# Kernel tuning notes

Measured on AMD Instinct MI355X. Metric: run time of the kernel, lower is better.

Reference implementation:

```python
import jax, jax.numpy as jnp
import numpy as np
from jax import lax

EPS = 1e-8
DIL = 4  # 2**(dilation-1) with dilation=3


def prelu(x, a):
    return jnp.where(x >= 0, x, a * x)


def cln(x):
    # cumulative layer norm over (channels, causal time window); gamma=1, beta=0
    # x: [B, M, L]
    M = x.shape[1]
    L = x.shape[2]
    cnt = (M * jnp.arange(1, L + 1, dtype=x.dtype))  # [L]
    csum = jnp.cumsum(jnp.sum(x, axis=1), axis=-1)           # [B, L]
    csq = jnp.cumsum(jnp.sum(x * x, axis=1), axis=-1)        # [B, L]
    mean = csum / cnt                                         # [B, L]
    var = csq / cnt - mean * mean                             # [B, L]
    return (x - mean[:, None, :]) / jnp.sqrt(var[:, None, :] + EPS)


def depthwise_conv(x, dw, db):
    # x: [B, H, L]; dw: [H, 1, P]; grouped conv, groups=H, 'same' padding, dilation DIL
    y = lax.conv_general_dilated(
        x, dw,
        window_strides=(1,),
        padding='SAME',
        rhs_dilation=(DIL,),
        dimension_numbers=('NCH', 'OIH', 'NCH'),
        feature_group_count=x.shape[1],
    )
    return y + db[None, :, None]


def setup_inputs() -> dict:
    key = jax.random.key(0)
    ks = jax.random.split(key, 9)
    Bc, H, P, Sc = 128, 512, 3, 128
    bsz, L = 4, 8000
    return {
        'x': jax.random.normal(ks[0], (bsz, Bc, L), dtype=jnp.float32),
        'W1': jax.random.normal(ks[1], (H, Bc), dtype=jnp.float32) * 0.05,
        'b1': jax.random.normal(ks[2], (H,), dtype=jnp.float32) * 0.02,
        'dw': jax.random.normal(ks[3], (H, 1, P), dtype=jnp.float32) * 0.1,
        'db': jax.random.normal(ks[4], (H,), dtype=jnp.float32) * 0.02,
        'Wout': jax.random.normal(ks[5], (Bc, H), dtype=jnp.float32) * 0.05,
        'bout': jax.random.normal(ks[6], (Bc,), dtype=jnp.float32) * 0.02,
        'Wskip': jax.random.normal(ks[7], (Sc, H), dtype=jnp.float32) * 0.05,
        'bskip': jax.random.normal(ks[8], (Sc,), dtype=jnp.float32) * 0.02,
        'a1': jnp.full((1,), 0.25, dtype=jnp.float32),
        'a2': jnp.full((1,), 0.25, dtype=jnp.float32),
    }


def reference(x, W1, b1, dw, db, Wout, bout, Wskip, bskip, a1, a2):
    res_x = x
    h = jnp.einsum('bcl,hc->bhl', x, W1) + b1[None, :, None]   # conv1x1 (k=1)
    h = prelu(h, a1)
    h = cln(h)
    h = depthwise_conv(h, dw, db)
    h = prelu(h, a2)
    h = cln(h)
    out = jnp.einsum('bhl,ch->bcl', h, Wout) + bout[None, :, None] + res_x
    skip = jnp.einsum('bhl,sh->bsl', h, Wskip) + bskip[None, :, None]
    return (out, skip)
```

## Files before the change

### kernel.cpp

```cpp
#include <hip/hip_runtime.h>

typedef unsigned short u16;
typedef unsigned int u32;
typedef __attribute__((ext_vector_type(8))) short bf16x8;
typedef __attribute__((ext_vector_type(4))) float f32x4;

#define Bn 4
#define Cn 128
#define Hn 512
#define Ln 8000
#define EPSf 1e-8f

__device__ __forceinline__ float bf2f(u32 v) { return __uint_as_float(v << 16); }
__device__ __forceinline__ u32 f2bf(float f) {
  u32 u = __float_as_uint(f);
  return (u + 0x7fffu + ((u >> 16) & 1u)) >> 16;
}
__device__ __forceinline__ void gl16(const void* g, void* l) {
  __builtin_amdgcn_global_load_lds((const __attribute__((address_space(1))) u32*)g,
                                   (__attribute__((address_space(3))) u32*)l, 16, 0, 0);
}

__global__ void k0_prep(const float* __restrict__ W1, const float* __restrict__ Wout,
                        const float* __restrict__ Wskip,
                        u16* __restrict__ W1b, u16* __restrict__ Wcatb,
                        float* __restrict__ Wsum)
{
  const int bid = blockIdx.x, tid = threadIdx.x;
  if (bid < 64) {
    const int base = (bid * 256 + tid) * 4;
#pragma unroll
    for (int t = 0; t < 4; ++t) {
      int i = base + t;
      int h = i >> 7, k = i & 127;
      int dbyte = h * 256 + (((k * 2) ^ ((h & 7) << 4)));
      W1b[dbyte >> 1] = (u16)f2bf(W1[h * Cn + k]);
    }
  } else if (bid < 192) {
    const int base = ((bid - 64) * 256 + tid) * 4;
#pragma unroll
    for (int t = 0; t < 4; ++t) {
      int j = base + t;
      int kt = j >> 14, r = j & 16383, c = r >> 6, kk = r & 63;
      int k = kt * 64 + kk;
      float v = (c < Cn) ? Wout[c * Hn + k] : Wskip[(c - Cn) * Hn + k];
      int dbyte = kt * 32768 + c * 128 + (((kk * 2) ^ ((c & 7) << 4)));
      Wcatb[dbyte >> 1] = (u16)f2bf(v);
    }
  } else {
    const int c = tid;
    const float* Wp = (c < Cn) ? (Wout + (size_t)c * Hn) : (Wskip + (size_t)(c - Cn) * Hn);
    float s = 0.f;
    for (int k = 0; k < Hn; ++k) s += Wp[k];
    Wsum[c] = s;
  }
}

__global__ __launch_bounds__(256, 2)
void k1_fused(const float* __restrict__ x, const u16* __restrict__ W1b,
              const float* __restrict__ b1, const float* __restrict__ a1p,
              u16* __restrict__ hT, float* __restrict__ sum1, float* __restrict__ sumsq1)
{
  __shared__ char regA[32768];
  __shared__ char xs[16384];
  __shared__ char stg[16384];
  __shared__ float b1s[512];
  const int bidx = blockIdx.x;
  const int b = bidx / 125, l0 = (bidx % 125) * 64;
  const int tid = threadIdx.x, ln = tid & 63, w = tid >> 6;
  const int ln15 = ln & 15, lq = ln >> 4;

  {
    const char* xb = (const char*)x + ((size_t)b * Cn * Ln + l0) * 4;
#pragma unroll
    for (int i = 0; i < 8; ++i) {
      int chunk = w * 8 + i;
      gl16(xb + (size_t)(chunk * 4 + (ln >> 4)) * (Ln * 4) + (ln & 15) * 16,
           regA + chunk * 1024);
    }
  }
  b1s[tid] = b1[tid];
  b1s[tid + 256] = b1[tid + 256];
  __syncthreads();
#pragma unroll
  for (int p = 0; p < 4; ++p) {
    int u = tid + p * 256;
    int l = u & 63, ui = u >> 6;
    u32 pk[4];
#pragma unroll
    for (int pp = 0; pp < 4; ++pp) {
      int c0 = ui * 8 + pp * 2;
      float f0 = *(const float*)(regA + c0 * 256 + l * 4);
      float f1 = *(const float*)(regA + (c0 + 1) * 256 + l * 4);
      pk[pp] = f2bf(f0) | (f2bf(f1) << 16);
    }
    uint4 st; st.x = pk[0]; st.y = pk[1]; st.z = pk[2]; st.w = pk[3];
    *(uint4*)(xs + l * 256 + ((ui * 16) ^ ((l & 7) << 4))) = st;
  }

  const float a1v = a1p[0];
  float sAcc = 0.f, qAcc = 0.f;

  for (int s = 0; s < 4; ++s) {
    __syncthreads();
#pragma unroll
    for (int i = 0; i < 8; ++i) {
      int chunk = w * 8 + i;
      gl16((const char*)W1b + s * 32768 + chunk * 1024 + ln * 16, regA + chunk * 1024);
    }
    __syncthreads();

    f32x4 acc[8];
    const f32x4 z4 = {0.f, 0.f, 0.f, 0.f};
#pragma unroll
    for (int rf = 0; rf < 8; ++rf) acc[rf] = z4;
#pragma unroll
    for (int kf = 0; kf < 4; ++kf) {
      const int brow = w * 16 + ln15;
      bf16x8 bfr = *(const bf16x8*)(xs + brow * 256 +
                                    ((kf * 64 + lq * 16) ^ ((brow & 7) << 4)));
#pragma unroll
      for (int rf = 0; rf < 8; ++rf) {
        int arow = rf * 16 + ln15;
        bf16x8 afr = *(const bf16x8*)(regA + arow * 256 +
                                      ((kf * 64 + lq * 16) ^ ((arow & 7) << 4)));
        acc[rf] = __builtin_amdgcn_mfma_f32_16x16x32_bf16(afr, bfr, acc[rf], 0, 0, 0);
      }
    }
#pragma unroll
    for (int rf = 0; rf < 8; ++rf) {
      int hb = s * 128 + rf * 16 + lq * 4;
      float v0 = acc[rf][0] + b1s[hb + 0]; v0 = v0 >= 0.f ? v0 : a1v * v0;
      float v1 = acc[rf][1] + b1s[hb + 1]; v1 = v1 >= 0.f ? v1 : a1v * v1;
      float v2 = acc[rf][2] + b1s[hb + 2]; v2 = v2 >= 0.f ? v2 : a1v * v2;
      float v3 = acc[rf][3] + b1s[hb + 3]; v3 = v3 >= 0.f ? v3 : a1v * v3;
      sAcc += v0 + v1 + v2 + v3;
      qAcc += v0 * v0 + v1 * v1 + v2 * v2 + v3 * v3;
      uint2 st2;
      st2.x = f2bf(v0) | (f2bf(v1) << 16);
      st2.y = f2bf(v2) | (f2bf(v3) << 16);
      *(uint2*)(stg + w * 4096 + ln15 * 256 +
                ((rf * 32 + lq * 8) ^ ((ln15 & 3) << 4))) = st2;
    }
#pragma unroll
    for (int p = 0; p < 4; ++p) {
      int lr = p * 4 + (ln >> 4);
      int j = ln & 15;
      uint4 v = *(const uint4*)(stg + w * 4096 + lr * 256 + ((j * 16) ^ ((lr & 3) << 4)));
      *(uint4*)((char*)hT + ((size_t)(b * Ln + l0 + w * 16 + lr)) * 1024 +
                s * 256 + j * 16) = v;
    }
  }
  sAcc += __shfl_xor(sAcc, 16); qAcc += __shfl_xor(qAcc, 16);
  sAcc += __shfl_xor(sAcc, 32); qAcc += __shfl_xor(qAcc, 32);
  if (lq == 0) {
    sum1[b * Ln + l0 + w * 16 + ln15] = sAcc;
    sumsq1[b * Ln + l0 + w * 16 + ln15] = qAcc;
  }
}

__global__ void k2_scan(const float* __restrict__ sum, const float* __restrict__ sumsq,
                        float* __restrict__ mean, float* __restrict__ rstd)
{
  const int b = blockIdx.x, tid = threadIdx.x;
  const int lane = tid & 63, w = tid >> 6;
  __shared__ float wts[4], wtq[4];
  float v[32], q[32];
  float ts = 0.f, tq = 0.f;
  const int base = tid * 32;
  const bool act = (tid < 250);
  if (act) {
#pragma unroll
    for (int i = 0; i < 8; ++i) {
      float4 a = *(const float4*)(sum + (size_t)b * Ln + base + i * 4);
      float4 c = *(const float4*)(sumsq + (size_t)b * Ln + base + i * 4);
      v[i * 4 + 0] = a.x; v[i * 4 + 1] = a.y; v[i * 4 + 2] = a.z; v[i * 4 + 3] = a.w;
      q[i * 4 + 0] = c.x; q[i * 4 + 1] = c.y; q[i * 4 + 2] = c.z; q[i * 4 + 3] = c.w;
    }
#pragma unroll
    for (int i = 0; i < 32; ++i) { ts += v[i]; tq += q[i]; }
  }
  float is = ts, iq = tq;
#pragma unroll
  for (int off = 1; off < 64; off <<= 1) {
    float a = __shfl_up(is, off);
    float c = __shfl_up(iq, off);
    if (lane >= off) { is += a; iq += c; }
  }
  float es = is - ts, eq = iq - tq;
  if (lane == 63) { wts[w] = is; wtq[w] = iq; }
  __syncthreads();
  for (int ww = 0; ww < w; ++ww) { es += wts[ww]; eq += wtq[ww]; }
  if (act) {
    float rs = es, rq = eq;
#pragma unroll
    for (int i = 0; i < 32; ++i) {
      rs += v[i]; rq += q[i];
      float cnt = 512.f * (float)(base + i + 1);
      float mn = rs / cnt;
      float var = fmaxf(rq / cnt - mn * mn, 0.f);
      v[i] = mn;
      q[i] = rsqrtf(var + EPSf);
    }
#pragma unroll
    for (int i = 0; i < 8; ++i) {
      float4 a; a.x = v[i*4+0]; a.y = v[i*4+1]; a.z = v[i*4+2]; a.w = v[i*4+3];
      float4 c; c.x = q[i*4+0]; c.y = q[i*4+1]; c.z = q[i*4+2]; c.w = q[i*4+3];
      *(float4*)(mean + (size_t)b * Ln + base + i * 4) = a;
      *(float4*)(rstd + (size_t)b * Ln + base + i * 4) = c;
    }
  }
}

__global__ __launch_bounds__(256, 2)
void k3_conv(const u16* __restrict__ hT, const float* __restrict__ mean1,
             const float* __restrict__ rstd1, const float* __restrict__ dw,
             const float* __restrict__ db, const float* __restrict__ a2p,
             u16* __restrict__ gT, float* __restrict__ sum2, float* __restrict__ sumsq2)
{
  __shared__ char hTs[73728];
  __shared__ float m1s[72], r1s[72];
  const int bidx = blockIdx.x;
  const int b = bidx / 125;
  const int l0 = (bidx % 125) * 64;
  const int tid = threadIdx.x;
  const int ln = tid & 63, w = tid >> 6;

  for (int i = 0; i < 18; ++i) {
    int chunk = w * 18 + i;
    int lr = l0 - 4 + chunk;
    int lc = lr < 0 ? 0 : (lr > Ln - 1 ? Ln - 1 : lr);
    gl16((const char*)hT + ((size_t)(b * Ln + lc)) * 1024 + ln * 16, hTs + chunk * 1024);
  }
  if (tid < 72) {
    int lr = l0 - 4 + tid;
    bool ok = (lr >= 0) && (lr < Ln);
    m1s[tid] = ok ? mean1[b * Ln + lr] : 0.f;
    r1s[tid] = ok ? rstd1[b * Ln + lr] : 0.f;
  }
  float d0[8], d1[8], d2[8], dbv[8];
#pragma unroll
  for (int e = 0; e < 8; ++e) {
    int hh = ln * 8 + e;
    d0[e] = dw[hh * 3 + 0]; d1[e] = dw[hh * 3 + 1]; d2[e] = dw[hh * 3 + 2];
    dbv[e] = db[hh];
  }
  const float a2v = a2p[0];
  __syncthreads();

  for (int it = 0; it < 16; ++it) {
    const int llo = w * 16 + it;
    const int l = l0 + llo;
    uint4 t0 = *reinterpret_cast<const uint4*>(hTs + (size_t)(llo) * 1024 + ln * 16);
    uint4 t1 = *reinterpret_cast<const uint4*>(hTs + (size_t)(llo + 4) * 1024 + ln * 16);
    uint4 t2 = *reinterpret_cast<const uint4*>(hTs + (size_t)(llo + 8) * 1024 + ln * 16);
    const float m0 = m1s[llo],     rr0 = r1s[llo];
    const float mC = m1s[llo + 4], rrC = r1s[llo + 4];
    const float m2v = m1s[llo + 8], rr2 = r1s[llo + 8];
    const u32* p0 = reinterpret_cast<const u32*>(&t0);
    const u32* p1 = reinterpret_cast<const u32*>(&t1);
    const u32* p2 = reinterpret_cast<const u32*>(&t2);
    float sv = 0.f, qv = 0.f;
    u32 outw[4];
#pragma unroll
    for (int pp = 0; pp < 4; ++pp) {
      float v01[2];
#pragma unroll
      for (int hi = 0; hi < 2; ++hi) {
        int e = pp * 2 + hi;
        u32 a0 = hi ? (p0[pp] >> 16) : (p0[pp] & 0xffffu);
        u32 a1b = hi ? (p1[pp] >> 16) : (p1[pp] & 0xffffu);
        u32 a2b = hi ? (p2[pp] >> 16) : (p2[pp] & 0xffffu);
        float nh0 = (bf2f(a0) - m0) * rr0;
        float nh1 = (bf2f(a1b) - mC) * rrC;
        float nh2 = (bf2f(a2b) - m2v) * rr2;
        float vv = fmaf(d0[e], nh0, fmaf(d1[e], nh1, fmaf(d2[e], nh2, dbv[e])));
        vv = vv >= 0.f ? vv : a2v * vv;
        sv += vv; qv += vv * vv;
        v01[hi] = vv;
      }
      outw[pp] = f2bf(v01[0]) | (f2bf(v01[1]) << 16);
    }
    uint4 st; st.x = outw[0]; st.y = outw[1]; st.z = outw[2]; st.w = outw[3];
    *reinterpret_cast<uint4*>((char*)gT + ((size_t)(b * Ln + l)) * 1024 +
                              (((ln * 16) ^ ((l & 7) << 4)))) = st;
#pragma unroll
    for (int off = 1; off < 64; off <<= 1) {
      sv += __shfl_xor(sv, off);
      qv += __shfl_xor(qv, off);
    }
    if (ln == 0) {
      sum2[b * Ln + l] = sv;
      sumsq2[b * Ln + l] = qv;
    }
  }
}

__global__ __launch_bounds__(256, 2)
void k5_gemm2(const u16* __restrict__ gT, const u16* __restrict__ Wcatb,
              const float* __restrict__ Wsum, const float* __restrict__ bout,
              const float* __restrict__ bskip, const float* __restrict__ mean2,
              const float* __restrict__ rstd2, const float* __restrict__ x,
              float* __restrict__ outp)
{
  __shared__ char Ab[2][32768];
  __shared__ char Bb[2][8192];
  const int bidx = blockIdx.x;
  const int b = bidx / 125;
  const int l0 = (bidx % 125) * 64;
  const int tid = threadIdx.x;
  const int ln = tid & 63, w = tid >> 6;
  const int ln15 = ln & 15, lq = ln >> 4;

  auto stage = [&](int kt, int bi) {
#pragma unroll
    for (int j = 0; j < 2; ++j) {
      int chunk = w * 2 + j;
      int lrow = chunk * 8 + (ln >> 3);
      int pos = (ln & 7) * 16;
      gl16((const char*)gT + ((size_t)(b * Ln + l0 + lrow)) * 1024 + kt * 128 + pos,
           Bb[bi] + chunk * 1024);
    }
    const char* Asrc = (const char*)Wcatb + kt * 32768;
#pragma unroll
    for (int i = 0; i < 8; ++i) {
      int chunk = w * 8 + i;
      gl16(Asrc + chunk * 1024 + ln * 16, Ab[bi] + chunk * 1024);
    }
  };

  f32x4 acc[4][4];
  const f32x4 z4 = {0.f, 0.f, 0.f, 0.f};
#pragma unroll
  for (int i = 0; i < 4; ++i)
#pragma unroll
    for (int j = 0; j < 4; ++j) acc[i][j] = z4;

  const int c0w = w * 64;
  stage(0, 0);
  __syncthreads();
  for (int kt = 0; kt < 8; ++kt) {
    const int cur = kt & 1;
    if (kt < 7) stage(kt + 1, cur ^ 1);
    const char* Ac = Ab[cur];
    const char* Bc = Bb[cur];
#pragma unroll
    for (int ks = 0; ks < 2; ++ks) {
      bf16x8 bfr[4];
#pragma unroll
      for (int cf = 0; cf < 4; ++cf) {
        int brow = cf * 16 + ln15;
        int off = ((ks * 64 + lq * 16) ^ ((brow & 7) << 4));
        bfr[cf] = *reinterpret_cast<const bf16x8*>(Bc + brow * 128 + off);
      }
#pragma unroll
      for (int rf = 0; rf < 4; ++rf) {
        int arow = c0w + rf * 16 + ln15;
        int aoff = ((ks * 64 + lq * 16) ^ ((arow & 7) << 4));
        bf16x8 afr = *reinterpret_cast<const bf16x8*>(Ac + arow * 128 + aoff);
#pragma unroll
        for (int cf = 0; cf < 4; ++cf)
          acc[rf][cf] = __builtin_amdgcn_mfma_f32_16x16x32_bf16(afr, bfr[cf], acc[rf][cf], 0, 0, 0);
      }
    }
    __syncthreads();
  }

  float wsr[4][4], bir[4][4];
#pragma unroll
  for (int rf = 0; rf < 4; ++rf)
#pragma unroll
    for (int r = 0; r < 4; ++r) {
      int c = c0w + rf * 16 + lq * 4 + r;
      wsr[rf][r] = Wsum[c];
      bir[rf][r] = (c < Cn) ? bout[c] : bskip[c - Cn];
    }
  const size_t OUTOFF = (size_t)Bn * Cn * Ln;
  char* stg = &Ab[0][0];
#pragma unroll
  for (int p = 0; p < 2; ++p) {
    if (p) __syncthreads();
#pragma unroll
    for (int cc = 0; cc < 2; ++cc) {
      const int cf = p * 2 + cc;
      const int ll = cc * 16 + ln15;
      const int l = l0 + cf * 16 + ln15;
      const float m2 = mean2[b * Ln + l];
      const float r2 = rstd2[b * Ln + l];
#pragma unroll
      for (int rf = 0; rf < 4; ++rf) {
#pragma unroll
        for (int r = 0; r < 4; ++r) {
          int c = c0w + rf * 16 + lq * 4 + r;
          float o = r2 * (acc[rf][cf][r] - m2 * wsr[rf][r]) + bir[rf][r];
          *(float*)(stg + c * 128 + ((((ll >> 2) ^ (c & 7)) << 4)) + (ll & 3) * 4) = o;
        }
      }
    }
    __syncthreads();
#pragma unroll
    for (int pp = 0; pp < 8; ++pp) {
      int i = pp * 256 + tid;
      int c = i >> 3, j = i & 7;
      float4 v = *(const float4*)(stg + c * 128 + (((j ^ (c & 7)) << 4)));
      int lcol = l0 + p * 32 + j * 4;
      if (c < Cn) {
        float4 xv = *(const float4*)(x + ((size_t)(b * Cn + c)) * Ln + lcol);
        v.x += xv.x; v.y += xv.y; v.z += xv.z; v.w += xv.w;
        *(float4*)(outp + ((size_t)(b * Cn + c)) * Ln + lcol) = v;
      } else {
        *(float4*)(outp + OUTOFF + ((size_t)(b * Cn + c - Cn)) * Ln + lcol) = v;
      }
    }
  }
}

extern "C" void kernel_launch(void* const* d_in, const int* in_sizes, int n_in,
                              void* d_out, int out_size, void* d_ws, size_t ws_size,
                              hipStream_t stream)
{
  const float* x     = (const float*)d_in[0];
  const float* W1    = (const float*)d_in[1];
  const float* b1    = (const float*)d_in[2];
  const float* dw    = (const float*)d_in[3];
  const float* db    = (const float*)d_in[4];
  const float* Wout  = (const float*)d_in[5];
  const float* bout  = (const float*)d_in[6];
  const float* Wskip = (const float*)d_in[7];
  const float* bskip = (const float*)d_in[8];
  const float* a1    = (const float*)d_in[9];
  const float* a2    = (const float*)d_in[10];
  float* outp = (float*)d_out;

  char* ws = (char*)d_ws;
  u16* hT     = (u16*)(ws);
  u16* gT     = (u16*)(ws + 32768000);
  u16* W1b    = (u16*)(ws + 65536000);
  u16* Wcatb  = (u16*)(ws + 65667072);
  float* Wsum   = (float*)(ws + 65929216);
  float* sum1   = (float*)(ws + 65930240);
  float* sumsq1 = (float*)(ws + 66058240);
  float* mean1  = (float*)(ws + 66186240);
  float* rstd1  = (float*)(ws + 66314240);
  float* sum2   = (float*)(ws + 66442240);
  float* sumsq2 = (float*)(ws + 66570240);
  float* mean2  = (float*)(ws + 66698240);
  float* rstd2  = (float*)(ws + 66826240);
  (void)in_sizes; (void)n_in; (void)out_size; (void)ws_size;

  hipLaunchKernelGGL(k0_prep, dim3(193), dim3(256), 0, stream,
                     W1, Wout, Wskip, W1b, Wcatb, Wsum);
  hipLaunchKernelGGL(k1_fused, dim3(Bn * 125), dim3(256), 0, stream,
                     x, W1b, b1, a1, hT, sum1, sumsq1);
  hipLaunchKernelGGL(k2_scan, dim3(Bn), dim3(256), 0, stream,
                     sum1, sumsq1, mean1, rstd1);
  hipLaunchKernelGGL(k3_conv, dim3(Bn * 125), dim3(256), 0, stream,
                     hT, mean1, rstd1, dw, db, a2, gT, sum2, sumsq2);
  hipLaunchKernelGGL(k2_scan, dim3(Bn), dim3(256), 0, stream,
                     sum2, sumsq2, mean2, rstd2);
  hipLaunchKernelGGL(k5_gemm2, dim3(Bn * 125), dim3(256), 0, stream,
                     gT, Wcatb, Wsum, bout, bskip, mean2, rstd2, x, outp);
}
```

Before: 94.20 us.

## Recompute depthwise conv inside output GEMM instead of materializing gT

The conv kernel now only produces per-timestep sums for the second cumulative layer norm and no longer writes the bf16 intermediate gT. The final GEMM kernel recomputes the depthwise conv and PReLU from hT into a 64KB shared tile, then runs the MFMA GEMM against it with 512 threads per block. This removes a 32MB write plus reread of gT, at the cost of reading hT twice and doing the conv arithmetic twice. It also lowers occupancy to one block per CU because of the larger shared memory use.

```diff
diff --git a/kernel.cpp b/kernel.cpp
--- a/kernel.cpp
+++ b/kernel.cpp
@@ -213,10 +213,10 @@
 }
 
 __global__ __launch_bounds__(256, 2)
-void k3_conv(const u16* __restrict__ hT, const float* __restrict__ mean1,
+void k3_sums(const u16* __restrict__ hT, const float* __restrict__ mean1,
              const float* __restrict__ rstd1, const float* __restrict__ dw,
              const float* __restrict__ db, const float* __restrict__ a2p,
-             u16* __restrict__ gT, float* __restrict__ sum2, float* __restrict__ sumsq2)
+             float* __restrict__ sum2, float* __restrict__ sumsq2)
 {
   __shared__ char hTs[73728];
   __shared__ float m1s[72], r1s[72];
@@ -261,10 +261,8 @@
     const u32* p1 = reinterpret_cast<const u32*>(&t1);
     const u32* p2 = reinterpret_cast<const u32*>(&t2);
     float sv = 0.f, qv = 0.f;
-    u32 outw[4];
 #pragma unroll
     for (int pp = 0; pp < 4; ++pp) {
-      float v01[2];
 #pragma unroll
       for (int hi = 0; hi < 2; ++hi) {
         int e = pp * 2 + hi;
@@ -277,13 +275,8 @@
         float vv = fmaf(d0[e], nh0, fmaf(d1[e], nh1, fmaf(d2[e], nh2, dbv[e])));
         vv = vv >= 0.f ? vv : a2v * vv;
         sv += vv; qv += vv * vv;
-        v01[hi] = vv;
       }
-      outw[pp] = f2bf(v01[0]) | (f2bf(v01[1]) << 16);
-    }
-    uint4 st; st.x = outw[0]; st.y = outw[1]; st.z = outw[2]; st.w = outw[3];
-    *reinterpret_cast<uint4*>((char*)gT + ((size_t)(b * Ln + l)) * 1024 +
-                              (((ln * 16) ^ ((l & 7) << 4)))) = st;
+    }
 #pragma unroll
     for (int off = 1; off < 64; off <<= 1) {
       sv += __shfl_xor(sv, off);
@@ -296,15 +289,19 @@
   }
 }
 
-__global__ __launch_bounds__(256, 2)
-void k5_gemm2(const u16* __restrict__ gT, const u16* __restrict__ Wcatb,
+__global__ __launch_bounds__(512, 1)
+void k5_fused(const u16* __restrict__ hT, const u16* __restrict__ Wcatb,
               const float* __restrict__ Wsum, const float* __restrict__ bout,
-              const float* __restrict__ bskip, const float* __restrict__ mean2,
-              const float* __restrict__ rstd2, const float* __restrict__ x,
-              float* __restrict__ outp)
+              const float* __restrict__ bskip,
+              const float* __restrict__ mean1, const float* __restrict__ rstd1,
+              const float* __restrict__ mean2, const float* __restrict__ rstd2,
+              const float* __restrict__ dw, const float* __restrict__ db,
+              const float* __restrict__ a2p,
+              const float* __restrict__ x, float* __restrict__ outp)
 {
+  __shared__ char Gb[65536];
   __shared__ char Ab[2][32768];
-  __shared__ char Bb[2][8192];
+  __shared__ float m1s[72], r1s[72], m2s[64], r2s[64];
   const int bidx = blockIdx.x;
   const int b = bidx / 125;
   const int l0 = (bidx % 125) * 64;
@@ -312,52 +309,104 @@
   const int ln = tid & 63, w = tid >> 6;
   const int ln15 = ln & 15, lq = ln >> 4;
 
-  auto stage = [&](int kt, int bi) {
-#pragma unroll
-    for (int j = 0; j < 2; ++j) {
-      int chunk = w * 2 + j;
-      int lrow = chunk * 8 + (ln >> 3);
-      int pos = (ln & 7) * 16;
-      gl16((const char*)gT + ((size_t)(b * Ln + l0 + lrow)) * 1024 + kt * 128 + pos,
-           Bb[bi] + chunk * 1024);
-    }
+  auto stageA = [&](int kt, int bi) {
     const char* Asrc = (const char*)Wcatb + kt * 32768;
 #pragma unroll
-    for (int i = 0; i < 8; ++i) {
-      int chunk = w * 8 + i;
+    for (int i = 0; i < 4; ++i) {
+      int chunk = w * 4 + i;
       gl16(Asrc + chunk * 1024 + ln * 16, Ab[bi] + chunk * 1024);
     }
   };
 
-  f32x4 acc[4][4];
+  stageA(0, 0);
+  uint4 t0[8], t1[8], t2[8];
+#pragma unroll
+  for (int it = 0; it < 8; ++it) {
+    const int l = l0 + w * 8 + it;
+    const int g0 = (l - 4 < 0) ? 0 : l - 4;
+    const int g2 = (l + 4 > Ln - 1) ? Ln - 1 : l + 4;
+    t0[it] = *(const uint4*)((const char*)hT + ((size_t)(b * Ln + g0)) * 1024 + ln * 16);
+    t1[it] = *(const uint4*)((const char*)hT + ((size_t)(b * Ln + l))  * 1024 + ln * 16);
+    t2[it] = *(const uint4*)((const char*)hT + ((size_t)(b * Ln + g2)) * 1024 + ln * 16);
+  }
+  float d0[8], d1[8], d2[8], dbv[8];
+#pragma unroll
+  for (int e = 0; e < 8; ++e) {
+    int hh = ln * 8 + e;
+    d0[e] = dw[hh * 3 + 0]; d1[e] = dw[hh * 3 + 1]; d2[e] = dw[hh * 3 + 2];
+    dbv[e] = db[hh];
+  }
+  if (tid < 72) {
+    int lr = l0 - 4 + tid;
+    bool ok = (lr >= 0) && (lr < Ln);
+    m1s[tid] = ok ? mean1[b * Ln + lr] : 0.f;
+    r1s[tid] = ok ? rstd1[b * Ln + lr] : 0.f;
+  }
+  if (tid < 64) {
+    m2s[tid] = mean2[b * Ln + l0 + tid];
+    r2s[tid] = rstd2[b * Ln + l0 + tid];
+  }
+  const float a2v = a2p[0];
+  __syncthreads();
+
+#pragma unroll
+  for (int it = 0; it < 8; ++it) {
+    const int llo = w * 8 + it;
+    const float m0 = m1s[llo],     rr0 = r1s[llo];
+    const float mC = m1s[llo + 4], rrC = r1s[llo + 4];
+    const float mB = m1s[llo + 8], rrB = r1s[llo + 8];
+    const u32* p0 = (const u32*)&t0[it];
+    const u32* p1 = (const u32*)&t1[it];
+    const u32* p2 = (const u32*)&t2[it];
+    u32 outw[4];
+#pragma unroll
+    for (int pp = 0; pp < 4; ++pp) {
+      float v01[2];
+#pragma unroll
+      for (int hi = 0; hi < 2; ++hi) {
+        int e = pp * 2 + hi;
+        u32 a0 = hi ? (p0[pp] >> 16) : (p0[pp] & 0xffffu);
+        u32 a1b = hi ? (p1[pp] >> 16) : (p1[pp] & 0xffffu);
+        u32 a2b = hi ? (p2[pp] >> 16) : (p2[pp] & 0xffffu);
+        float nh0 = (bf2f(a0) - m0) * rr0;
+        float nh1 = (bf2f(a1b) - mC) * rrC;
+        float nh2 = (bf2f(a2b) - mB) * rrB;
+        float vv = fmaf(d0[e], nh0, fmaf(d1[e], nh1, fmaf(d2[e], nh2, dbv[e])));
+        v01[hi] = vv >= 0.f ? vv : a2v * vv;
+      }
+      outw[pp] = f2bf(v01[0]) | (f2bf(v01[1]) << 16);
+    }
+    uint4 st; st.x = outw[0]; st.y = outw[1]; st.z = outw[2]; st.w = outw[3];
+    *(uint4*)(Gb + llo * 1024 + ((ln & 56) << 4) +
+              ((((ln & 7) ^ (llo & 7))) << 4)) = st;
+  }
+  __syncthreads();
+
+  f32x4 acc[2][4];
   const f32x4 z4 = {0.f, 0.f, 0.f, 0.f};
 #pragma unroll
-  for (int i = 0; i < 4; ++i)
+  for (int i = 0; i < 2; ++i)
 #pragma unroll
     for (int j = 0; j < 4; ++j) acc[i][j] = z4;
-
-  const int c0w = w * 64;
-  stage(0, 0);
-  __syncthreads();
+  const int c0w = w * 32;
+
   for (int kt = 0; kt < 8; ++kt) {
     const int cur = kt & 1;
-    if (kt < 7) stage(kt + 1, cur ^ 1);
-    const char* Ac = Ab[cur];
-    const char* Bc = Bb[cur];
+    if (kt < 7) stageA(kt + 1, cur ^ 1);
 #pragma unroll
     for (int ks = 0; ks < 2; ++ks) {
       bf16x8 bfr[4];
 #pragma unroll
       for (int cf = 0; cf < 4; ++cf) {
         int brow = cf * 16 + ln15;
-        int off = ((ks * 64 + lq * 16) ^ ((brow & 7) << 4));
-        bfr[cf] = *reinterpret_cast<const bf16x8*>(Bc + brow * 128 + off);
+        bfr[cf] = *(const bf16x8*)(Gb + brow * 1024 + kt * 128 +
+                                   ((ks * 64 + lq * 16) ^ ((brow & 7) << 4)));
       }
 #pragma unroll
-      for (int rf = 0; rf < 4; ++rf) {
+      for (int rf = 0; rf < 2; ++rf) {
         int arow = c0w + rf * 16 + ln15;
-        int aoff = ((ks * 64 + lq * 16) ^ ((arow & 7) << 4));
-        bf16x8 afr = *reinterpret_cast<const bf16x8*>(Ac + arow * 128 + aoff);
+        bf16x8 afr = *(const bf16x8*)(Ab[cur] + arow * 128 +
+                                      ((ks * 64 + lq * 16) ^ ((arow & 7) << 4)));
 #pragma unroll
         for (int cf = 0; cf < 4; ++cf)
           acc[rf][cf] = __builtin_amdgcn_mfma_f32_16x16x32_bf16(afr, bfr[cf], acc[rf][cf], 0, 0, 0);
@@ -366,51 +415,44 @@
     __syncthreads();
   }
 
-  float wsr[4][4], bir[4][4];
-#pragma unroll
-  for (int rf = 0; rf < 4; ++rf)
+  float wsr[2][4], bir[2][4];
+#pragma unroll
+  for (int rf = 0; rf < 2; ++rf)
 #pragma unroll
     for (int r = 0; r < 4; ++r) {
       int c = c0w + rf * 16 + lq * 4 + r;
       wsr[rf][r] = Wsum[c];
       bir[rf][r] = (c < Cn) ? bout[c] : bskip[c - Cn];
     }
+#pragma unroll
+  for (int cf = 0; cf < 4; ++cf) {
+    const int ll = cf * 16 + ln15;
+    const float m2 = m2s[ll];
+    const float r2 = r2s[ll];
+#pragma unroll
+    for (int rf = 0; rf < 2; ++rf) {
+#pragma unroll
+      for (int r = 0; r < 4; ++r) {
+        int c = c0w + rf * 16 + lq * 4 + r;
+        float o = r2 * (acc[rf][cf][r] - m2 * wsr[rf][r]) + bir[rf][r];
+        *(float*)(Gb + c * 256 + ((((ll >> 2) ^ (c & 7)) << 4)) + (ll & 3) * 4) = o;
+      }
+    }
+  }
+  __syncthreads();
   const size_t OUTOFF = (size_t)Bn * Cn * Ln;
-  char* stg = &Ab[0][0];
-#pragma unroll
-  for (int p = 0; p < 2; ++p) {
-    if (p) __syncthreads();
-#pragma unroll
-    for (int cc = 0; cc < 2; ++cc) {
-      const int cf = p * 2 + cc;
-      const int ll = cc * 16 + ln15;
-      const int l = l0 + cf * 16 + ln15;
-      const float m2 = mean2[b * Ln + l];
-      const float r2 = rstd2[b * Ln + l];
-#pragma unroll
-      for (int rf = 0; rf < 4; ++rf) {
-#pragma unroll
-        for (int r = 0; r < 4; ++r) {
-          int c = c0w + rf * 16 + lq * 4 + r;
-          float o = r2 * (acc[rf][cf][r] - m2 * wsr[rf][r]) + bir[rf][r];
-          *(float*)(stg + c * 128 + ((((ll >> 2) ^ (c & 7)) << 4)) + (ll & 3) * 4) = o;
-        }
-      }
-    }
-    __syncthreads();
-#pragma unroll
-    for (int pp = 0; pp < 8; ++pp) {
-      int i = pp * 256 + tid;
-      int c = i >> 3, j = i & 7;
-      float4 v = *(const float4*)(stg + c * 128 + (((j ^ (c & 7)) << 4)));
-      int lcol = l0 + p * 32 + j * 4;
-      if (c < Cn) {
-        float4 xv = *(const float4*)(x + ((size_t)(b * Cn + c)) * Ln + lcol);
-        v.x += xv.x; v.y += xv.y; v.z += xv.z; v.w += xv.w;
-        *(float4*)(outp + ((size_t)(b * Cn + c)) * Ln + lcol) = v;
-      } else {
-        *(float4*)(outp + OUTOFF + ((size_t)(b * Cn + c - Cn)) * Ln + lcol) = v;
-      }
+#pragma unroll
+  for (int pp = 0; pp < 8; ++pp) {
+    int i = pp * 512 + tid;
+    int c = i >> 4, j = i & 15;
+    float4 v = *(const float4*)(Gb + c * 256 + (((j ^ (c & 7)) << 4)));
+    int lcol = l0 + j * 4;
+    if (c < Cn) {
+      float4 xv = *(const float4*)(x + ((size_t)(b * Cn + c)) * Ln + lcol);
+      v.x += xv.x; v.y += xv.y; v.z += xv.z; v.w += xv.w;
+      *(float4*)(outp + ((size_t)(b * Cn + c)) * Ln + lcol) = v;
+    } else {
+      *(float4*)(outp + OUTOFF + ((size_t)(b * Cn + c - Cn)) * Ln + lcol) = v;
     }
   }
 }
@@ -434,7 +476,6 @@
 
   char* ws = (char*)d_ws;
   u16* hT     = (u16*)(ws);
-  u16* gT     = (u16*)(ws + 32768000);
   u16* W1b    = (u16*)(ws + 65536000);
   u16* Wcatb  = (u16*)(ws + 65667072);
   float* Wsum   = (float*)(ws + 65929216);
@@ -454,10 +495,11 @@
                      x, W1b, b1, a1, hT, sum1, sumsq1);
   hipLaunchKernelGGL(k2_scan, dim3(Bn), dim3(256), 0, stream,
                      sum1, sumsq1, mean1, rstd1);
-  hipLaunchKernelGGL(k3_conv, dim3(Bn * 125), dim3(256), 0, stream,
-                     hT, mean1, rstd1, dw, db, a2, gT, sum2, sumsq2);
+  hipLaunchKernelGGL(k3_sums, dim3(Bn * 125), dim3(256), 0, stream,
+                     hT, mean1, rstd1, dw, db, a2, sum2, sumsq2);
   hipLaunchKernelGGL(k2_scan, dim3(Bn), dim3(256), 0, stream,
                      sum2, sumsq2, mean2, rstd2);
-  hipLaunchKernelGGL(k5_gemm2, dim3(Bn * 125), dim3(256), 0, stream,
-                     gT, Wcatb, Wsum, bout, bskip, mean2, rstd2, x, outp);
-}
+  hipLaunchKernelGGL(k5_fused, dim3(Bn * 125), dim3(512), 0, stream,
+                     hT, Wcatb, Wsum, bout, bskip, mean1, rstd1, mean2, rstd2,
+                     dw, db, a2, x, outp);
+}
```

Result: slower. 103.0 us (+9.4%).

## Replace LDS-staged depthwise conv with direct global loads and smaller tiles

Applied to the files above, without the earlier changes.

The depthwise conv kernel no longer stages a 72-row halo tile of hT into 72KB of shared memory. Each thread now loads its three dilated taps and their norm statistics straight from global memory, relying on cache for reuse. The tile shrinks to 32 positions per block, the grid doubles and launch bounds rise to 4 blocks per SM, aiming for higher occupancy and no LDS barrier. The cost is about three times as many global reads, served from L2. The GEMM2 staging lambda also issues the weight loads before the activation loads.

```diff
diff --git a/kernel.cpp b/kernel.cpp
--- a/kernel.cpp
+++ b/kernel.cpp
@@ -212,32 +212,18 @@
   }
 }
 
-__global__ __launch_bounds__(256, 2)
-void k3_conv(const u16* __restrict__ hT, const float* __restrict__ mean1,
-             const float* __restrict__ rstd1, const float* __restrict__ dw,
-             const float* __restrict__ db, const float* __restrict__ a2p,
-             u16* __restrict__ gT, float* __restrict__ sum2, float* __restrict__ sumsq2)
-{
-  __shared__ char hTs[73728];
-  __shared__ float m1s[72], r1s[72];
+__global__ __launch_bounds__(256, 4)
+void k3_direct(const u16* __restrict__ hT, const float* __restrict__ mean1,
+               const float* __restrict__ rstd1, const float* __restrict__ dw,
+               const float* __restrict__ db, const float* __restrict__ a2p,
+               u16* __restrict__ gT, float* __restrict__ sum2, float* __restrict__ sumsq2)
+{
   const int bidx = blockIdx.x;
-  const int b = bidx / 125;
-  const int l0 = (bidx % 125) * 64;
+  const int b = bidx / 250;
+  const int l0 = (bidx % 250) * 32;
   const int tid = threadIdx.x;
   const int ln = tid & 63, w = tid >> 6;
 
-  for (int i = 0; i < 18; ++i) {
-    int chunk = w * 18 + i;
-    int lr = l0 - 4 + chunk;
-    int lc = lr < 0 ? 0 : (lr > Ln - 1 ? Ln - 1 : lr);
-    gl16((const char*)hT + ((size_t)(b * Ln + lc)) * 1024 + ln * 16, hTs + chunk * 1024);
-  }
-  if (tid < 72) {
-    int lr = l0 - 4 + tid;
-    bool ok = (lr >= 0) && (lr < Ln);
-    m1s[tid] = ok ? mean1[b * Ln + lr] : 0.f;
-    r1s[tid] = ok ? rstd1[b * Ln + lr] : 0.f;
-  }
   float d0[8], d1[8], d2[8], dbv[8];
 #pragma unroll
   for (int e = 0; e < 8; ++e) {
@@ -246,17 +232,22 @@
     dbv[e] = db[hh];
   }
   const float a2v = a2p[0];
-  __syncthreads();
-
-  for (int it = 0; it < 16; ++it) {
-    const int llo = w * 16 + it;
-    const int l = l0 + llo;
-    uint4 t0 = *reinterpret_cast<const uint4*>(hTs + (size_t)(llo) * 1024 + ln * 16);
-    uint4 t1 = *reinterpret_cast<const uint4*>(hTs + (size_t)(llo + 4) * 1024 + ln * 16);
-    uint4 t2 = *reinterpret_cast<const uint4*>(hTs + (size_t)(llo + 8) * 1024 + ln * 16);
-    const float m0 = m1s[llo],     rr0 = r1s[llo];
-    const float mC = m1s[llo + 4], rrC = r1s[llo + 4];
-    const float m2v = m1s[llo + 8], rr2 = r1s[llo + 8];
+  const char* hTb = (const char*)hT + (size_t)b * Ln * 1024;
+
+#pragma unroll
+  for (int it = 0; it < 8; ++it) {
+    const int l = l0 + w * 8 + it;
+    const int g0 = l - 4, g2 = l + 4;
+    const bool ok0 = (g0 >= 0), ok2 = (g2 < Ln);
+    uint4 t0 = *(const uint4*)(hTb + (size_t)(ok0 ? g0 : 0) * 1024 + ln * 16);
+    uint4 t1 = *(const uint4*)(hTb + (size_t)l * 1024 + ln * 16);
+    uint4 t2 = *(const uint4*)(hTb + (size_t)(ok2 ? g2 : Ln - 1) * 1024 + ln * 16);
+    const float m0 = ok0 ? mean1[b * Ln + g0] : 0.f;
+    const float rr0 = ok0 ? rstd1[b * Ln + g0] : 0.f;
+    const float mC = mean1[b * Ln + l];
+    const float rrC = rstd1[b * Ln + l];
+    const float mB = ok2 ? mean1[b * Ln + g2] : 0.f;
+    const float rrB = ok2 ? rstd1[b * Ln + g2] : 0.f;
     const u32* p0 = reinterpret_cast<const u32*>(&t0);
     const u32* p1 = reinterpret_cast<const u32*>(&t1);
     const u32* p2 = reinterpret_cast<const u32*>(&t2);
@@ -273,7 +264,7 @@
         u32 a2b = hi ? (p2[pp] >> 16) : (p2[pp] & 0xffffu);
         float nh0 = (bf2f(a0) - m0) * rr0;
         float nh1 = (bf2f(a1b) - mC) * rrC;
-        float nh2 = (bf2f(a2b) - m2v) * rr2;
+        float nh2 = (bf2f(a2b) - mB) * rrB;
         float vv = fmaf(d0[e], nh0, fmaf(d1[e], nh1, fmaf(d2[e], nh2, dbv[e])));
         vv = vv >= 0.f ? vv : a2v * vv;
         sv += vv; qv += vv * vv;
@@ -313,6 +304,12 @@
   const int ln15 = ln & 15, lq = ln >> 4;
 
   auto stage = [&](int kt, int bi) {
+    const char* Asrc = (const char*)Wcatb + kt * 32768;
+#pragma unroll
+    for (int i = 0; i < 8; ++i) {
+      int chunk = w * 8 + i;
+      gl16(Asrc + chunk * 1024 + ln * 16, Ab[bi] + chunk * 1024);
+    }
 #pragma unroll
     for (int j = 0; j < 2; ++j) {
       int chunk = w * 2 + j;
@@ -320,12 +317,6 @@
       int pos = (ln & 7) * 16;
       gl16((const char*)gT + ((size_t)(b * Ln + l0 + lrow)) * 1024 + kt * 128 + pos,
            Bb[bi] + chunk * 1024);
-    }
-    const char* Asrc = (const char*)Wcatb + kt * 32768;
-#pragma unroll
-    for (int i = 0; i < 8; ++i) {
-      int chunk = w * 8 + i;
-      gl16(Asrc + chunk * 1024 + ln * 16, Ab[bi] + chunk * 1024);
     }
   };
 
@@ -454,7 +445,7 @@
                      x, W1b, b1, a1, hT, sum1, sumsq1);
   hipLaunchKernelGGL(k2_scan, dim3(Bn), dim3(256), 0, stream,
                      sum1, sumsq1, mean1, rstd1);
-  hipLaunchKernelGGL(k3_conv, dim3(Bn * 125), dim3(256), 0, stream,
+  hipLaunchKernelGGL(k3_direct, dim3(Bn * 250), dim3(256), 0, stream,
                      hT, mean1, rstd1, dw, db, a2, gT, sum2, sumsq2);
   hipLaunchKernelGGL(k2_scan, dim3(Bn), dim3(256), 0, stream,
                      sum2, sumsq2, mean2, rstd2);
```

New measurement: 93.24 us. Within noise of the previous version (-1.0%).
